# Optimization experiments

Measured on AMD Instinct MI355X. Metric: run time of the kernel, lower is better.

The kernel has to match this reference:

```python
import jax, jax.numpy as jnp
import numpy as np

HID = 128
N_USER = 50000
N_MERCH = 50000
D_IN = 64


def _glorot(key, shape):
    fan_in = shape[1]
    return jax.random.normal(key, shape, dtype=jnp.float32) / jnp.sqrt(jnp.float32(fan_in))


def _sage(x_src, x_dst, ei, Wl, bl, Wr, n_dst):
    # PyG SAGEConv: lin_l(mean_aggr(x_j)) + lin_r(x_dst)
    row, col = ei[0], ei[1]
    agg = jax.ops.segment_sum(x_src[row], col, num_segments=n_dst)
    cnt = jax.ops.segment_sum(jnp.ones((ei.shape[1],), x_src.dtype), col, num_segments=n_dst)
    mean = agg / jnp.maximum(cnt, 1.0)[:, None]
    return mean @ Wl.T + bl + x_dst @ Wr.T


def setup_inputs() -> dict:
    key = jax.random.key(0)
    ks = jax.random.split(key, 24)
    inp = {
        "x_user": jax.random.normal(ks[0], (N_USER, D_IN), dtype=jnp.float32),
        "x_merchant": jax.random.normal(ks[1], (N_MERCH, D_IN), dtype=jnp.float32),
        "edge_um": jax.random.randint(ks[2], (2, 1000000), 0, 50000, dtype=jnp.int64),
        "edge_mu": jax.random.randint(ks[3], (2, 1000000), 0, 50000, dtype=jnp.int64),
        "target_edge_index": jax.random.randint(ks[4], (2, 500000), 0, 50000, dtype=jnp.int64),
        # layer 1, edge type user->merchant (src=user D_IN, dst=merchant D_IN)
        "W1_um_l": _glorot(ks[5], (HID, D_IN)), "b1_um_l": jnp.zeros((HID,), jnp.float32),
        "W1_um_r": _glorot(ks[6], (HID, D_IN)),
        # layer 1, edge type merchant->user
        "W1_mu_l": _glorot(ks[7], (HID, D_IN)), "b1_mu_l": jnp.zeros((HID,), jnp.float32),
        "W1_mu_r": _glorot(ks[8], (HID, D_IN)),
        # layer 2 (hidden -> hidden)
        "W2_um_l": _glorot(ks[9], (HID, HID)), "b2_um_l": jnp.zeros((HID,), jnp.float32),
        "W2_um_r": _glorot(ks[10], (HID, HID)),
        "W2_mu_l": _glorot(ks[11], (HID, HID)), "b2_mu_l": jnp.zeros((HID,), jnp.float32),
        "W2_mu_r": _glorot(ks[12], (HID, HID)),
        # edge classifier MLP
        "Wc1": _glorot(ks[13], (HID, 2 * HID)), "bc1": jnp.zeros((HID,), jnp.float32),
        "Wc2": _glorot(ks[14], (1, HID)), "bc2": jnp.zeros((1,), jnp.float32),
    }
    return inp


def reference(x_user, x_merchant, edge_um, edge_mu, target_edge_index,
              W1_um_l, b1_um_l, W1_um_r, W1_mu_l, b1_mu_l, W1_mu_r,
              W2_um_l, b2_um_l, W2_um_r, W2_mu_l, b2_mu_l, W2_mu_r,
              Wc1, bc1, Wc2, bc2):
    # layer 1 (to_hetero: each dst type aggregates its single incoming edge type)
    h_m = jax.nn.relu(_sage(x_user, x_merchant, edge_um, W1_um_l, b1_um_l, W1_um_r, N_MERCH))
    h_u = jax.nn.relu(_sage(x_merchant, x_user, edge_mu, W1_mu_l, b1_mu_l, W1_mu_r, N_USER))
    # layer 2 (no relu)
    z_m = _sage(h_u, h_m, edge_um, W2_um_l, b2_um_l, W2_um_r, N_MERCH)
    z_u = _sage(h_m, h_u, edge_mu, W2_mu_l, b2_mu_l, W2_mu_r, N_USER)
    # edge classifier: sender_type='user', receiver_type='merchant'
    row, col = target_edge_index[0], target_edge_index[1]
    z = jnp.concatenate([z_u[row], z_m[col]], axis=-1)  # [E_t, 2*HID]
    z = jax.nn.relu(z @ Wc1.T + bc1)
    z = z @ Wc2.T + bc2
    return z.reshape(-1)
```

## Files before the change

### kernel.cpp

```cpp
#include <hip/hip_runtime.h>
#include <hip/hip_bf16.h>
#include <stdint.h>

#define N_USERC  50000
#define N_MERCHC 50000
#define NEC      1000000
#define NTC      500000

#define NB    196
#define BCAP  8192
#define ECHUNK 2048
#define BPT   489

#define PREP_BKT   (2 * BPT)
#define PREP_CASTX (PREP_BKT + 3125)
#define PREP_CASTW (PREP_CASTX + 16)
#define PREP_TOT   (PREP_CASTW + 257)

typedef unsigned short ushortT;
typedef __attribute__((ext_vector_type(8))) short short8;
typedef __attribute__((ext_vector_type(8))) unsigned short ushort8;
typedef __attribute__((ext_vector_type(4))) float f32x4;
typedef __attribute__((ext_vector_type(2))) float f32x2;

__device__ __forceinline__ unsigned short f2bf(float f)
{
    const unsigned u = __float_as_uint(f);
    const unsigned r = u + 0x7fffu + ((u >> 16) & 1u);
    return (unsigned short)(r >> 16);
}
__device__ __forceinline__ float bfhi(unsigned u) { return __uint_as_float(u & 0xffff0000u); }
__device__ __forceinline__ float bflo(unsigned u) { return __uint_as_float(u << 16); }

__device__ __forceinline__ void acc8p(f32x2* a, const uint4 v)
{
    a[0] += (f32x2){bflo(v.x), bfhi(v.x)};
    a[1] += (f32x2){bflo(v.y), bfhi(v.y)};
    a[2] += (f32x2){bflo(v.z), bfhi(v.z)};
    a[3] += (f32x2){bflo(v.w), bfhi(v.w)};
}

__global__ __launch_bounds__(256) void k_prep(
    const float* __restrict__ xu, const float* __restrict__ xm,
    ushortT* __restrict__ A1u, ushortT* __restrict__ A1m,
    const float* __restrict__ W1um_l, const float* __restrict__ W1um_r,
    const float* __restrict__ W1mu_l, const float* __restrict__ W1mu_r,
    ushortT* __restrict__ B1m, ushortT* __restrict__ B1u,
    const float* __restrict__ Wc1,
    const float* __restrict__ W2mu_l, const float* __restrict__ W2mu_r,
    const float* __restrict__ W2um_l, const float* __restrict__ W2um_r,
    const float* __restrict__ bc1,
    const float* __restrict__ b2mu_l, const float* __restrict__ b2um_l,
    ushortT* __restrict__ WPQ, float* __restrict__ bPQ,
    const int* __restrict__ rowA, const int* __restrict__ colA,
    const int* __restrict__ rowB, const int* __restrict__ colB,
    uint32_t* __restrict__ gcnt, uint32_t* __restrict__ bktA, uint32_t* __restrict__ bktB)
{
    __shared__ uint32_t hist[NB], base[NB], cur[NB];
    const int bid = blockIdx.x;
    const int tx = threadIdx.x;

    if (bid < PREP_BKT) {
        const int type = (bid >= BPT) ? 1 : 0;
        const int cb = bid - type * BPT;
        const int* col = type ? colB : colA;
        const int* row = type ? rowB : rowA;
        uint32_t* bkt = type ? bktB : bktA;
        uint32_t* gc = gcnt + type * NB;

        const int e0 = cb * ECHUNK;
        const int e1 = (e0 + ECHUNK < NEC) ? e0 + ECHUNK : NEC;

        for (int i = tx; i < NB; i += 256) { hist[i] = 0; cur[i] = 0; }
        __syncthreads();

        int cols[8];
#pragma unroll
        for (int q = 0; q < 8; ++q) {
            const int i = e0 + tx + q * 256;
            int c = -1;
            if (i < e1) { c = col[i]; atomicAdd(&hist[c >> 8], 1u); }
            cols[q] = c;
        }
        __syncthreads();
        for (int i = tx; i < NB; i += 256)
            base[i] = atomicAdd(&gc[i], hist[i]);
        __syncthreads();
#pragma unroll
        for (int q = 0; q < 8; ++q) {
            const int i = e0 + tx + q * 256;
            if (i < e1) {
                const int c = cols[q];
                const int b = c >> 8;
                const uint32_t p = base[b] + atomicAdd(&cur[b], 1u);
                if (p < BCAP)
                    bkt[(size_t)b * BCAP + p] = ((uint32_t)(c & 255) << 16) | (uint32_t)row[i];
            }
        }
    } else if (bid < PREP_CASTX) {
        const int idx = (bid - PREP_BKT) * 256 + tx;
        if (idx >= 800000) return;
        const int which = idx / 400000;
        const int rem = idx - which * 400000;
        const int row = rem >> 3;
        const int c8 = rem & 7;
        const float* x = which ? xm : xu;
        ushortT* A = which ? A1m : A1u;
        const float4 v0 = *(const float4*)(x + (size_t)row * 64 + c8 * 8);
        const float4 v1 = *(const float4*)(x + (size_t)row * 64 + c8 * 8 + 4);
        ushort8 o;
        o[0] = f2bf(v0.x); o[1] = f2bf(v0.y); o[2] = f2bf(v0.z); o[3] = f2bf(v0.w);
        o[4] = f2bf(v1.x); o[5] = f2bf(v1.y); o[6] = f2bf(v1.z); o[7] = f2bf(v1.w);
        *(ushort8*)(A + (size_t)row * 128 + 64 + c8 * 8) = o;
    } else if (bid < PREP_CASTW) {
        const int idx = (bid - PREP_CASTX) * 256 + tx;
        if (idx >= 4096) return;
        const int which = idx >> 11;
        const int rem = idx & 2047;
        const int n = rem >> 4;
        const int k0 = (rem & 15) * 8;
        const float* Wl = which ? W1mu_l : W1um_l;
        const float* Wr = which ? W1mu_r : W1um_r;
        const float* src = (k0 < 64) ? Wl + (size_t)n * 64 + k0
                                     : Wr + (size_t)n * 64 + (k0 - 64);
        const float4 v0 = *(const float4*)src;
        const float4 v1 = *(const float4*)(src + 4);
        ushort8 o;
        o[0] = f2bf(v0.x); o[1] = f2bf(v0.y); o[2] = f2bf(v0.z); o[3] = f2bf(v0.w);
        o[4] = f2bf(v1.x); o[5] = f2bf(v1.y); o[6] = f2bf(v1.z); o[7] = f2bf(v1.w);
        ushortT* O = which ? B1u : B1m;
        *(ushort8*)(O + (size_t)n * 128 + k0) = o;
    } else {
        const int idx = (bid - PREP_CASTW) * 256 + tx;
        if (idx < 65536) {
            const int q = idx >> 15;
            const int j = (idx >> 8) & 127;
            const int k = idx & 255;
            const int kk = k & 127;
            const float* W2 = q ? (k < 128 ? W2um_l : W2um_r)
                                : (k < 128 ? W2mu_l : W2mu_r);
            const float* wrow = Wc1 + (size_t)j * 256 + q * 128;
            float s = 0.f;
            for (int i = 0; i < 128; ++i)
                s = fmaf(wrow[i], W2[(size_t)i * 128 + kk], s);
            WPQ[idx] = f2bf(s);
        } else if (idx < 65536 + 256) {
            const int r = idx - 65536;
            const int q = r >> 7, j = r & 127;
            const float* wrow = Wc1 + (size_t)j * 256 + q * 128;
            const float* b2 = q ? b2um_l : b2mu_l;
            float s = (q == 0) ? bc1[j] : 0.f;
            for (int i = 0; i < 128; ++i) s = fmaf(wrow[i], b2[i], s);
            bPQ[r] = s;
        }
    }
}

__global__ __launch_bounds__(512) void k_bplace(
    const uint32_t* __restrict__ gcnt,
    const uint32_t* __restrict__ bktA, const uint32_t* __restrict__ bktB,
    int* __restrict__ off_um, int* __restrict__ srcs_um,
    int* __restrict__ off_mu, int* __restrict__ srcs_mu)
{
    __shared__ uint32_t sb[256], cnt[256], loff[256], cur[256];
    const int type = (blockIdx.x >= NB) ? 1 : 0;
    const int b = blockIdx.x - type * NB;
    const uint32_t* bkt = (type ? bktB : bktA) + (size_t)b * BCAP;
    int* offp = type ? off_mu : off_um;
    int* srcs = type ? srcs_mu : srcs_um;
    const int t = threadIdx.x;

    if (t < 256) sb[t] = (t < NB) ? gcnt[type * NB + t] : 0;
    for (int d = 1; d < 256; d <<= 1) {
        __syncthreads();
        uint32_t a = 0;
        if (t < 256 && t >= d) a = sb[t - d];
        __syncthreads();
        if (t < 256) sb[t] += a;
    }
    __syncthreads();
    const int n = (int)gcnt[type * NB + b];
    const uint32_t gbase = sb[b] - (uint32_t)n;
    if (blockIdx.x == 0 && t == 0)  off_um[N_MERCHC] = NEC;
    if (blockIdx.x == NB && t == 0) off_mu[N_USERC] = NEC;

    if (t < 256) { cnt[t] = 0; cur[t] = 0; }
    __syncthreads();
    for (int i = t; i < n; i += 512)
        atomicAdd(&cnt[bkt[i] >> 16], 1u);
    __syncthreads();
    if (t < 256) loff[t] = cnt[t];
    for (int d = 1; d < 256; d <<= 1) {
        __syncthreads();
        uint32_t a = 0;
        if (t < 256 && t >= d) a = loff[t - d];
        __syncthreads();
        if (t < 256) loff[t] += a;
    }
    __syncthreads();
    if (t < 256) loff[t] -= cnt[t];
    __syncthreads();
    if (t < 256) {
        const int dst0 = b << 8;
        if (dst0 + t < N_USERC) offp[dst0 + t] = (int)(gbase + loff[t]);
    }
    for (int i = t; i < n; i += 512) {
        const uint32_t v = bkt[i];
        const uint32_t ld = v >> 16;
        const uint32_t p = gbase + loff[ld] + atomicAdd(&cur[ld], 1u);
        srcs[p] = (int)(v & 0xFFFFu);
    }
}

template <int D>
__global__ __launch_bounds__(256) void k_agg(
    const ushortT* __restrict__ gA, const int* __restrict__ offsA,
    const int* __restrict__ srcsA, ushortT* __restrict__ oA,
    const ushortT* __restrict__ gB, const int* __restrict__ offsB,
    const int* __restrict__ srcsB, ushortT* __restrict__ oB, int ndst)
{
    constexpr int LPE = D / 8;
    constexpr int EPW = 64 / LPE;
    constexpr int UNR = (D == 128) ? 8 : 4;
    constexpr int STR = 2 * D;
    constexpr unsigned RB = 4 * D;
    const int half = gridDim.x >> 1;
    const int type = (blockIdx.x >= half) ? 1 : 0;
    const int cb = blockIdx.x - type * half;
    const ushortT* g = type ? gB : gA;
    const int* offs  = type ? offsB : offsA;
    const int* srcs  = type ? srcsB : srcsA;
    ushortT* om      = type ? oB : oA;

    const int wid = cb * 4 + (threadIdx.x >> 6);
    if (wid >= ndst) return;
    const int lane = threadIdx.x & 63;
    const int sub  = lane / LPE;
    const int c4   = lane % LPE;

    const int b = offs[wid], e = offs[wid + 1];
    const int deg = e - b;
    const char* gDc = (const char*)(g + D) + c4 * 16;

    f32x2 a0[4], a1[4];
#pragma unroll
    for (int j = 0; j < 4; ++j) { a0[j] = (f32x2){0.f, 0.f}; a1[j] = (f32x2){0.f, 0.f}; }

    if (deg <= 64) {
        const int sidx = (b + lane < NEC) ? b + lane : NEC - 1;
        const int src_l = srcs[sidx];
        for (int t0 = 0; t0 < deg; t0 += UNR * EPW) {
            uint4 v[UNR];
#pragma unroll
            for (int r = 0; r < UNR; ++r) {
                const int j = t0 + r * EPW + sub;
                const int s = __shfl(src_l, j);
                v[r] = (uint4){0u, 0u, 0u, 0u};
                if (j < deg)
                    v[r] = *(const uint4*)(gDc + (unsigned)s * RB);
            }
            __builtin_amdgcn_sched_barrier(0);
#pragma unroll
            for (int r = 0; r < UNR; ++r)
                acc8p((r & 1) ? a1 : a0, v[r]);
        }
    } else {
        int i = b + sub;
        for (; i + EPW < e; i += 2 * EPW) {
            const uint4 v0 = *(const uint4*)(gDc + (unsigned)srcs[i] * RB);
            const uint4 v1 = *(const uint4*)(gDc + (unsigned)srcs[i + EPW] * RB);
            acc8p(a0, v0);
            acc8p(a1, v1);
        }
        if (i < e) {
            const uint4 v = *(const uint4*)(gDc + (unsigned)srcs[i] * RB);
            acc8p(a0, v);
        }
    }

    float r[8];
#pragma unroll
    for (int j = 0; j < 4; ++j) {
        r[2 * j]     = a0[j].x + a1[j].x;
        r[2 * j + 1] = a0[j].y + a1[j].y;
    }
#pragma unroll
    for (int m = LPE; m < 64; m <<= 1) {
#pragma unroll
        for (int j = 0; j < 8; ++j) r[j] += __shfl_xor(r[j], m);
    }
    if (sub == 0) {
        const float inv = 1.0f / (float)(deg > 1 ? deg : 1);
        ushort8 o;
#pragma unroll
        for (int j = 0; j < 8; ++j) o[j] = f2bf(r[j] * inv);
        *(ushort8*)(om + (size_t)wid * STR + c4 * 8) = o;
    }
}

template <int K, bool RELU>
__device__ __forceinline__ void mfma_gemm_body(
    int cb, float (*lds)[16][132],
    const ushortT* __restrict__ A, const ushortT* __restrict__ Bw,
    const float* __restrict__ bias,
    ushortT* __restrict__ Obf, int OS, int OO, int M)
{
    const int tx = threadIdx.x;
    const int wid = tx >> 6;
    const int lane = tx & 63;
    const int ln = lane & 15;
    const int quad = lane >> 4;
    const int m0 = cb * 256 + wid * 64;

    const ushortT* ap[4];
#pragma unroll
    for (int i = 0; i < 4; ++i) {
        int arow = m0 + i * 16 + ln; if (arow >= M) arow = M - 1;
        ap[i] = A + (size_t)arow * K + quad * 8;
    }

    f32x4 acc[4][8];
#pragma unroll
    for (int i = 0; i < 4; ++i)
#pragma unroll
        for (int nt = 0; nt < 8; ++nt) acc[i][nt] = (f32x4){0.f, 0.f, 0.f, 0.f};

#pragma unroll
    for (int kc = 0; kc < K / 32; ++kc) {
        short8 a[4];
#pragma unroll
        for (int i = 0; i < 4; ++i) a[i] = *(const short8*)(ap[i] + kc * 32);
#pragma unroll
        for (int nt = 0; nt < 8; ++nt) {
            const short8 b = *(const short8*)(Bw + (size_t)(nt * 16 + ln) * K + kc * 32 + quad * 8);
#pragma unroll
            for (int i = 0; i < 4; ++i)
                acc[i][nt] = __builtin_amdgcn_mfma_f32_16x16x32_bf16(a[i], b, acc[i][nt], 0, 0, 0);
        }
    }

    float (*t)[132] = lds[wid];
#pragma unroll
    for (int i = 0; i < 4; ++i) {
#pragma unroll
        for (int nt = 0; nt < 8; ++nt) {
            const float bv = bias[nt * 16 + ln];
#pragma unroll
            for (int r = 0; r < 4; ++r) {
                float v = acc[i][nt][r] + bv;
                if (RELU) v = fmaxf(v, 0.f);
                t[quad * 4 + r][nt * 16 + ln] = v;
            }
        }
#pragma unroll
        for (int p = 0; p < 4; ++p) {
            const int row = p * 4 + quad;
            const int gr = m0 + i * 16 + row;
            if (gr < M) {
                const float4 v0 = *(const float4*)&t[row][ln * 8];
                const float4 v1 = *(const float4*)&t[row][ln * 8 + 4];
                ushort8 o;
                o[0] = f2bf(v0.x); o[1] = f2bf(v0.y); o[2] = f2bf(v0.z); o[3] = f2bf(v0.w);
                o[4] = f2bf(v1.x); o[5] = f2bf(v1.y); o[6] = f2bf(v1.z); o[7] = f2bf(v1.w);
                *(ushort8*)(Obf + (size_t)gr * OS + OO + ln * 8) = o;
            }
        }
    }
}

template <int K, bool RELU>
__global__ __launch_bounds__(256) void k_mfma_gemm2(
    const ushortT* __restrict__ Aa, const ushortT* __restrict__ Bwa,
    const float* __restrict__ biasa, ushortT* __restrict__ Oa, int OSa, int OOa, int Ma,
    const ushortT* __restrict__ Ab, const ushortT* __restrict__ Bwb,
    const float* __restrict__ biasb, ushortT* __restrict__ Ob, int OSb, int OOb, int Mb,
    int gridA)
{
    __shared__ float lds[4][16][132];
    if ((int)blockIdx.x < gridA)
        mfma_gemm_body<K, RELU>(blockIdx.x, lds, Aa, Bwa, biasa, Oa, OSa, OOa, Ma);
    else
        mfma_gemm_body<K, RELU>(blockIdx.x - gridA, lds, Ab, Bwb, biasb, Ob, OSb, OOb, Mb);
}

__global__ __launch_bounds__(256) void k_edge_bf(
    const ushortT* __restrict__ P, const ushortT* __restrict__ Q,
    const int* __restrict__ er, const int* __restrict__ ec,
    const float* __restrict__ wc2, const float* __restrict__ bc2,
    float* __restrict__ out, int nt)
{
    const int lane = threadIdx.x & 63;
    const int sub = lane >> 4;
    const int c8 = lane & 15;
    const int wid = (int)((blockIdx.x * blockDim.x + threadIdx.x) >> 6);
    const int e0 = wid * 4 + sub;
    if (e0 >= nt) return;

    const float4 w0 = ((const float4*)wc2)[c8 * 2];
    const float4 w1 = ((const float4*)wc2)[c8 * 2 + 1];
    const int r = er[e0], c = ec[e0];
    const uint4 pv = *(const uint4*)(P + (size_t)r * 128 + c8 * 8);
    const uint4 qv = *(const uint4*)(Q + (size_t)c * 128 + c8 * 8);
    float s = fmaxf(bflo(pv.x) + bflo(qv.x), 0.f) * w0.x
            + fmaxf(bfhi(pv.x) + bfhi(qv.x), 0.f) * w0.y
            + fmaxf(bflo(pv.y) + bflo(qv.y), 0.f) * w0.z
            + fmaxf(bfhi(pv.y) + bfhi(qv.y), 0.f) * w0.w
            + fmaxf(bflo(pv.z) + bflo(qv.z), 0.f) * w1.x
            + fmaxf(bfhi(pv.z) + bfhi(qv.z), 0.f) * w1.y
            + fmaxf(bflo(pv.w) + bflo(qv.w), 0.f) * w1.z
            + fmaxf(bfhi(pv.w) + bfhi(qv.w), 0.f) * w1.w;
    s += __shfl_xor(s, 1);
    s += __shfl_xor(s, 2);
    s += __shfl_xor(s, 4);
    s += __shfl_xor(s, 8);
    if (c8 == 0) out[e0] = s + bc2[0];
}

extern "C" void kernel_launch(void* const* d_in, const int* in_sizes, int n_in,
                              void* d_out, int out_size, void* d_ws, size_t ws_size,
                              hipStream_t stream)
{
    const float* x_user  = (const float*)d_in[0];
    const float* x_merch = (const float*)d_in[1];
    const int*   e_um    = (const int*)d_in[2];
    const int*   e_mu    = (const int*)d_in[3];
    const int*   tgt     = (const int*)d_in[4];
    const float* W1_um_l = (const float*)d_in[5];
    const float* b1_um_l = (const float*)d_in[6];
    const float* W1_um_r = (const float*)d_in[7];
    const float* W1_mu_l = (const float*)d_in[8];
    const float* b1_mu_l = (const float*)d_in[9];
    const float* W1_mu_r = (const float*)d_in[10];
    const float* W2_um_l = (const float*)d_in[11];
    const float* b2_um_l = (const float*)d_in[12];
    const float* W2_um_r = (const float*)d_in[13];
    const float* W2_mu_l = (const float*)d_in[14];
    const float* b2_mu_l = (const float*)d_in[15];
    const float* W2_mu_r = (const float*)d_in[16];
    const float* Wc1     = (const float*)d_in[17];
    const float* bc1     = (const float*)d_in[18];
    const float* Wc2     = (const float*)d_in[19];
    const float* bc2     = (const float*)d_in[20];
    float* out = (float*)d_out;

    uint32_t* B = (uint32_t*)d_ws;
    size_t pos = 0;
    auto take = [&](size_t n) { size_t p = pos; pos += (n + 63) & ~(size_t)63; return p; };

    uint32_t* gcnt = (uint32_t*)(B + take(2 * NB));
    const size_t cnt_words = pos;
    int* off_um  = (int*)(B + take(N_MERCHC + 1));
    int* srcs_um = (int*)(B + take(NEC));
    int* off_mu  = (int*)(B + take(N_USERC + 1));
    int* srcs_mu = (int*)(B + take(NEC));
    ushortT* A1u = (ushortT*)(B + take((size_t)N_USERC  * 128 / 2));
    ushortT* A1m = (ushortT*)(B + take((size_t)N_MERCHC * 128 / 2));
    ushortT* A2u = (ushortT*)(B + take((size_t)N_USERC  * 256 / 2));
    ushortT* A2m = (ushortT*)(B + take((size_t)N_MERCHC * 256 / 2));
    ushortT* B1m = (ushortT*)(B + take(8192));
    ushortT* B1u = (ushortT*)(B + take(8192));
    ushortT* WPQ = (ushortT*)(B + take(32768));
    float*   bPQ = (float*)(B + take(256));

    uint32_t* bktA = (uint32_t*)A2m;
    uint32_t* bktB = bktA + (size_t)NB * BCAP;
    ushortT* Pbf = A1u;
    ushortT* Qbf = A1m;
    (void)ws_size; (void)in_sizes; (void)n_in; (void)out_size;

    hipMemsetAsync(d_ws, 0, cnt_words * sizeof(uint32_t), stream);

    k_prep<<<PREP_TOT, 256, 0, stream>>>(
        x_user, x_merch, A1u, A1m,
        W1_um_l, W1_um_r, W1_mu_l, W1_mu_r, B1m, B1u,
        Wc1, W2_mu_l, W2_mu_r, W2_um_l, W2_um_r, bc1, b2_mu_l, b2_um_l, WPQ, bPQ,
        e_um, e_um + NEC, e_mu, e_mu + NEC, gcnt, bktA, bktB);

    k_bplace<<<2 * NB, 512, 0, stream>>>(gcnt, bktA, bktB,
                                         off_um, srcs_um, off_mu, srcs_mu);

    const int agrid = 50000 / 4;
    k_agg<64><<<2 * agrid, 256, 0, stream>>>(
        A1u, off_um, srcs_um, A1m,
        A1m, off_mu, srcs_mu, A1u, N_MERCHC);

    const int ggrid = (50000 + 255) / 256;
    k_mfma_gemm2<128, true><<<2 * ggrid, 256, 0, stream>>>(
        A1m, B1m, b1_um_l, A2m, 256, 128, N_MERCHC,
        A1u, B1u, b1_mu_l, A2u, 256, 128, N_USERC, ggrid);

    k_agg<128><<<2 * agrid, 256, 0, stream>>>(
        A2u, off_um, srcs_um, A2m,
        A2m, off_mu, srcs_mu, A2u, N_MERCHC);

    k_mfma_gemm2<256, false><<<2 * ggrid, 256, 0, stream>>>(
        A2u, WPQ,         bPQ,       Pbf, 128, 0, N_USERC,
        A2m, WPQ + 32768, bPQ + 128, Qbf, 128, 0, N_MERCHC, ggrid);

    const int cgrid = (NTC + 15) / 16;
    k_edge_bf<<<cgrid, 256, 0, stream>>>(Pbf, Qbf, tgt, tgt + NTC, Wc2, bc2, out, NTC);
}
```

Measured before the change: 348.5 us.

## Bucket target edges by user into CSR so edge classifier reuses P rows

```diff
diff --git a/kernel.cpp b/kernel.cpp
--- a/kernel.cpp
+++ b/kernel.cpp
@@ -9,10 +9,12 @@
 
 #define NB    196
 #define BCAP  8192
+#define TCAP  4096
 #define ECHUNK 2048
 #define BPT   489
-
-#define PREP_BKT   (2 * BPT)
+#define BPTT  245
+
+#define PREP_BKT   (2 * BPT + BPTT)
 #define PREP_CASTX (PREP_BKT + 3125)
 #define PREP_CASTW (PREP_CASTX + 16)
 #define PREP_TOT   (PREP_CASTW + 257)
@@ -38,6 +40,19 @@
     a[1] += (f32x2){bflo(v.y), bfhi(v.y)};
     a[2] += (f32x2){bflo(v.z), bfhi(v.z)};
     a[3] += (f32x2){bflo(v.w), bfhi(v.w)};
+}
+
+__device__ __forceinline__ float edot8(const uint4 pv, const uint4 qv,
+                                       const float4 w0, const float4 w1)
+{
+    return fmaxf(bflo(pv.x) + bflo(qv.x), 0.f) * w0.x
+         + fmaxf(bfhi(pv.x) + bfhi(qv.x), 0.f) * w0.y
+         + fmaxf(bflo(pv.y) + bflo(qv.y), 0.f) * w0.z
+         + fmaxf(bfhi(pv.y) + bfhi(qv.y), 0.f) * w0.w
+         + fmaxf(bflo(pv.z) + bflo(qv.z), 0.f) * w1.x
+         + fmaxf(bfhi(pv.z) + bfhi(qv.z), 0.f) * w1.y
+         + fmaxf(bflo(pv.w) + bflo(qv.w), 0.f) * w1.z
+         + fmaxf(bfhi(pv.w) + bfhi(qv.w), 0.f) * w1.w;
 }
 
 __global__ __launch_bounds__(256) void k_prep(
@@ -54,22 +69,26 @@
     ushortT* __restrict__ WPQ, float* __restrict__ bPQ,
     const int* __restrict__ rowA, const int* __restrict__ colA,
     const int* __restrict__ rowB, const int* __restrict__ colB,
-    uint32_t* __restrict__ gcnt, uint32_t* __restrict__ bktA, uint32_t* __restrict__ bktB)
+    const int* __restrict__ tgr, const int* __restrict__ tgc,
+    uint32_t* __restrict__ gcnt, uint32_t* __restrict__ bktA, uint32_t* __restrict__ bktB,
+    uint32_t* __restrict__ bktTlo, uint32_t* __restrict__ bktThi)
 {
     __shared__ uint32_t hist[NB], base[NB], cur[NB];
     const int bid = blockIdx.x;
     const int tx = threadIdx.x;
 
     if (bid < PREP_BKT) {
-        const int type = (bid >= BPT) ? 1 : 0;
-        const int cb = bid - type * BPT;
-        const int* col = type ? colB : colA;
-        const int* row = type ? rowB : rowA;
-        uint32_t* bkt = type ? bktB : bktA;
+        const int type = (bid >= 2 * BPT) ? 2 : (bid >= BPT ? 1 : 0);
+        const int cb = bid - (type == 2 ? 2 * BPT : type * BPT);
+        const int* col = (type == 2) ? tgr : (type ? colB : colA);
+        const int* row = (type == 2) ? tgc : (type ? rowB : rowA);
+        uint32_t* bklo = (type == 2) ? bktTlo : (type ? bktB : bktA);
         uint32_t* gc = gcnt + type * NB;
+        const int nE  = (type == 2) ? NTC : NEC;
+        const int cap = (type == 2) ? TCAP : BCAP;
 
         const int e0 = cb * ECHUNK;
-        const int e1 = (e0 + ECHUNK < NEC) ? e0 + ECHUNK : NEC;
+        const int e1 = (e0 + ECHUNK < nE) ? e0 + ECHUNK : nE;
 
         for (int i = tx; i < NB; i += 256) { hist[i] = 0; cur[i] = 0; }
         __syncthreads();
@@ -93,8 +112,11 @@
                 const int c = cols[q];
                 const int b = c >> 8;
                 const uint32_t p = base[b] + atomicAdd(&cur[b], 1u);
-                if (p < BCAP)
-                    bkt[(size_t)b * BCAP + p] = ((uint32_t)(c & 255) << 16) | (uint32_t)row[i];
+                if (p < (uint32_t)cap) {
+                    const uint32_t idx = (uint32_t)b * cap + p;
+                    bklo[idx] = ((uint32_t)(c & 255) << 16) | (uint32_t)row[i];
+                    if (type == 2) bktThi[idx] = (uint32_t)i;
+                }
             }
         }
     } else if (bid < PREP_CASTX) {
@@ -159,15 +181,17 @@
 __global__ __launch_bounds__(512) void k_bplace(
     const uint32_t* __restrict__ gcnt,
     const uint32_t* __restrict__ bktA, const uint32_t* __restrict__ bktB,
+    const uint32_t* __restrict__ bktTlo, const uint32_t* __restrict__ bktThi,
     int* __restrict__ off_um, int* __restrict__ srcs_um,
-    int* __restrict__ off_mu, int* __restrict__ srcs_mu)
+    int* __restrict__ off_mu, int* __restrict__ srcs_mu,
+    int* __restrict__ offT, int2* __restrict__ payT)
 {
     __shared__ uint32_t sb[256], cnt[256], loff[256], cur[256];
-    const int type = (blockIdx.x >= NB) ? 1 : 0;
+    const int type = (blockIdx.x >= 2 * NB) ? 2 : (blockIdx.x >= NB ? 1 : 0);
     const int b = blockIdx.x - type * NB;
-    const uint32_t* bkt = (type ? bktB : bktA) + (size_t)b * BCAP;
-    int* offp = type ? off_mu : off_um;
-    int* srcs = type ? srcs_mu : srcs_um;
+    const int cap = (type == 2) ? TCAP : BCAP;
+    const uint32_t* bkt = ((type == 2) ? bktTlo : (type ? bktB : bktA)) + (size_t)b * cap;
+    int* offp = (type == 2) ? offT : (type ? off_mu : off_um);
     const int t = threadIdx.x;
 
     if (t < 256) sb[t] = (t < NB) ? gcnt[type * NB + t] : 0;
@@ -181,8 +205,9 @@
     __syncthreads();
     const int n = (int)gcnt[type * NB + b];
     const uint32_t gbase = sb[b] - (uint32_t)n;
-    if (blockIdx.x == 0 && t == 0)  off_um[N_MERCHC] = NEC;
-    if (blockIdx.x == NB && t == 0) off_mu[N_USERC] = NEC;
+    if (blockIdx.x == 0 && t == 0)      off_um[N_MERCHC] = NEC;
+    if (blockIdx.x == NB && t == 0)     off_mu[N_USERC] = NEC;
+    if (blockIdx.x == 2 * NB && t == 0) offT[N_USERC] = NTC;
 
     if (t < 256) { cnt[t] = 0; cur[t] = 0; }
     __syncthreads();
@@ -204,11 +229,22 @@
         const int dst0 = b << 8;
         if (dst0 + t < N_USERC) offp[dst0 + t] = (int)(gbase + loff[t]);
     }
-    for (int i = t; i < n; i += 512) {
-        const uint32_t v = bkt[i];
-        const uint32_t ld = v >> 16;
-        const uint32_t p = gbase + loff[ld] + atomicAdd(&cur[ld], 1u);
-        srcs[p] = (int)(v & 0xFFFFu);
+    if (type < 2) {
+        int* srcs = type ? srcs_mu : srcs_um;
+        for (int i = t; i < n; i += 512) {
+            const uint32_t v = bkt[i];
+            const uint32_t ld = v >> 16;
+            const uint32_t p = gbase + loff[ld] + atomicAdd(&cur[ld], 1u);
+            srcs[p] = (int)(v & 0xFFFFu);
+        }
+    } else {
+        const uint32_t* hi = bktThi + (size_t)b * cap;
+        for (int i = t; i < n; i += 512) {
+            const uint32_t v = bkt[i];
+            const uint32_t ld = v >> 16;
+            const uint32_t p = gbase + loff[ld] + atomicAdd(&cur[ld], 1u);
+            payT[p] = (int2){(int)(v & 0xFFFFu), (int)hi[i]};
+        }
     }
 }
 
@@ -383,37 +419,36 @@
         mfma_gemm_body<K, RELU>(blockIdx.x - gridA, lds, Ab, Bwb, biasb, Ob, OSb, OOb, Mb);
 }
 
-__global__ __launch_bounds__(256) void k_edge_bf(
+__global__ __launch_bounds__(256) void k_edge_csr(
     const ushortT* __restrict__ P, const ushortT* __restrict__ Q,
-    const int* __restrict__ er, const int* __restrict__ ec,
+    const int* __restrict__ offT, const int2* __restrict__ payT,
     const float* __restrict__ wc2, const float* __restrict__ bc2,
-    float* __restrict__ out, int nt)
-{
+    float* __restrict__ out)
+{
+    const int wid = (int)((blockIdx.x * blockDim.x + threadIdx.x) >> 6);
+    if (wid >= N_USERC) return;
     const int lane = threadIdx.x & 63;
     const int sub = lane >> 4;
     const int c8 = lane & 15;
-    const int wid = (int)((blockIdx.x * blockDim.x + threadIdx.x) >> 6);
-    const int e0 = wid * 4 + sub;
-    if (e0 >= nt) return;
+
+    const int b = offT[wid], e = offT[wid + 1];
+    if (b == e) return;
 
     const float4 w0 = ((const float4*)wc2)[c8 * 2];
     const float4 w1 = ((const float4*)wc2)[c8 * 2 + 1];
-    const int r = er[e0], c = ec[e0];
-    const uint4 pv = *(const uint4*)(P + (size_t)r * 128 + c8 * 8);
-    const uint4 qv = *(const uint4*)(Q + (size_t)c * 128 + c8 * 8);
-    float s = fmaxf(bflo(pv.x) + bflo(qv.x), 0.f) * w0.x
-            + fmaxf(bfhi(pv.x) + bfhi(qv.x), 0.f) * w0.y
-            + fmaxf(bflo(pv.y) + bflo(qv.y), 0.f) * w0.z
-            + fmaxf(bfhi(pv.y) + bfhi(qv.y), 0.f) * w0.w
-            + fmaxf(bflo(pv.z) + bflo(qv.z), 0.f) * w1.x
-            + fmaxf(bfhi(pv.z) + bfhi(qv.z), 0.f) * w1.y
-            + fmaxf(bflo(pv.w) + bflo(qv.w), 0.f) * w1.z
-            + fmaxf(bfhi(pv.w) + bfhi(qv.w), 0.f) * w1.w;
-    s += __shfl_xor(s, 1);
-    s += __shfl_xor(s, 2);
-    s += __shfl_xor(s, 4);
-    s += __shfl_xor(s, 8);
-    if (c8 == 0) out[e0] = s + bc2[0];
+    const float bb = bc2[0];
+    const uint4 pv = *(const uint4*)(P + (size_t)wid * 128 + c8 * 8);
+
+    for (int i = b + sub; i < e; i += 4) {
+        const int2 pe = payT[i];
+        const uint4 qv = *(const uint4*)(Q + (size_t)pe.x * 128 + c8 * 8);
+        float s = edot8(pv, qv, w0, w1);
+        s += __shfl_xor(s, 1);
+        s += __shfl_xor(s, 2);
+        s += __shfl_xor(s, 4);
+        s += __shfl_xor(s, 8);
+        if (c8 == 0) out[pe.y] = s + bb;
+    }
 }
 
 extern "C" void kernel_launch(void* const* d_in, const int* in_sizes, int n_in,
@@ -447,12 +482,14 @@
     size_t pos = 0;
     auto take = [&](size_t n) { size_t p = pos; pos += (n + 63) & ~(size_t)63; return p; };
 
-    uint32_t* gcnt = (uint32_t*)(B + take(2 * NB));
+    uint32_t* gcnt = (uint32_t*)(B + take(3 * NB));
     const size_t cnt_words = pos;
     int* off_um  = (int*)(B + take(N_MERCHC + 1));
     int* srcs_um = (int*)(B + take(NEC));
     int* off_mu  = (int*)(B + take(N_USERC + 1));
     int* srcs_mu = (int*)(B + take(NEC));
+    int* offT    = (int*)(B + take(N_USERC + 1));
+    int2* payT   = (int2*)(B + take(2 * (size_t)NTC));
     ushortT* A1u = (ushortT*)(B + take((size_t)N_USERC  * 128 / 2));
     ushortT* A1m = (ushortT*)(B + take((size_t)N_MERCHC * 128 / 2));
     ushortT* A2u = (ushortT*)(B + take((size_t)N_USERC  * 256 / 2));
@@ -462,8 +499,10 @@
     ushortT* WPQ = (ushortT*)(B + take(32768));
     float*   bPQ = (float*)(B + take(256));
 
-    uint32_t* bktA = (uint32_t*)A2m;
-    uint32_t* bktB = bktA + (size_t)NB * BCAP;
+    uint32_t* bktA   = (uint32_t*)A2m;
+    uint32_t* bktB   = bktA + (size_t)NB * BCAP;
+    uint32_t* bktTlo = bktB + (size_t)NB * BCAP;
+    uint32_t* bktThi = bktTlo + (size_t)NB * TCAP;
     ushortT* Pbf = A1u;
     ushortT* Qbf = A1m;
     (void)ws_size; (void)in_sizes; (void)n_in; (void)out_size;
@@ -474,10 +513,11 @@
         x_user, x_merch, A1u, A1m,
         W1_um_l, W1_um_r, W1_mu_l, W1_mu_r, B1m, B1u,
         Wc1, W2_mu_l, W2_mu_r, W2_um_l, W2_um_r, bc1, b2_mu_l, b2_um_l, WPQ, bPQ,
-        e_um, e_um + NEC, e_mu, e_mu + NEC, gcnt, bktA, bktB);
-
-    k_bplace<<<2 * NB, 512, 0, stream>>>(gcnt, bktA, bktB,
-                                         off_um, srcs_um, off_mu, srcs_mu);
+        e_um, e_um + NEC, e_mu, e_mu + NEC, tgt, tgt + NTC,
+        gcnt, bktA, bktB, bktTlo, bktThi);
+
+    k_bplace<<<3 * NB, 512, 0, stream>>>(gcnt, bktA, bktB, bktTlo, bktThi,
+                                         off_um, srcs_um, off_mu, srcs_mu, offT, payT);
 
     const int agrid = 50000 / 4;
     k_agg<64><<<2 * agrid, 256, 0, stream>>>(
@@ -497,6 +537,6 @@
         A2u, WPQ,         bPQ,       Pbf, 128, 0, N_USERC,
         A2m, WPQ + 32768, bPQ + 128, Qbf, 128, 0, N_MERCHC, ggrid);
 
-    const int cgrid = (NTC + 15) / 16;
-    k_edge_bf<<<cgrid, 256, 0, stream>>>(Pbf, Qbf, tgt, tgt + NTC, Wc2, bc2, out, NTC);
-}
+    const int cgrid = (N_USERC + 3) / 4;
+    k_edge_csr<<<cgrid, 256, 0, stream>>>(Pbf, Qbf, offT, payT, Wc2, bc2, out);
+}
```

After: 362.7 us. 1.04x slower.

## Bucket target edges by user row to localize classifier gathers

Applied to the files above, without the earlier changes.

```diff
diff --git a/kernel.cpp b/kernel.cpp
--- a/kernel.cpp
+++ b/kernel.cpp
@@ -9,10 +9,12 @@
 
 #define NB    196
 #define BCAP  8192
+#define TCAP  4096
 #define ECHUNK 2048
 #define BPT   489
-
-#define PREP_BKT   (2 * BPT)
+#define BPTT  245
+
+#define PREP_BKT   (2 * BPT + BPTT)
 #define PREP_CASTX (PREP_BKT + 3125)
 #define PREP_CASTW (PREP_CASTX + 16)
 #define PREP_TOT   (PREP_CASTW + 257)
@@ -38,6 +40,19 @@
     a[1] += (f32x2){bflo(v.y), bfhi(v.y)};
     a[2] += (f32x2){bflo(v.z), bfhi(v.z)};
     a[3] += (f32x2){bflo(v.w), bfhi(v.w)};
+}
+
+__device__ __forceinline__ float edot8(const uint4 pv, const uint4 qv,
+                                       const float4 w0, const float4 w1)
+{
+    return fmaxf(bflo(pv.x) + bflo(qv.x), 0.f) * w0.x
+         + fmaxf(bfhi(pv.x) + bfhi(qv.x), 0.f) * w0.y
+         + fmaxf(bflo(pv.y) + bflo(qv.y), 0.f) * w0.z
+         + fmaxf(bfhi(pv.y) + bfhi(qv.y), 0.f) * w0.w
+         + fmaxf(bflo(pv.z) + bflo(qv.z), 0.f) * w1.x
+         + fmaxf(bfhi(pv.z) + bfhi(qv.z), 0.f) * w1.y
+         + fmaxf(bflo(pv.w) + bflo(qv.w), 0.f) * w1.z
+         + fmaxf(bfhi(pv.w) + bfhi(qv.w), 0.f) * w1.w;
 }
 
 __global__ __launch_bounds__(256) void k_prep(
@@ -54,22 +69,26 @@
     ushortT* __restrict__ WPQ, float* __restrict__ bPQ,
     const int* __restrict__ rowA, const int* __restrict__ colA,
     const int* __restrict__ rowB, const int* __restrict__ colB,
-    uint32_t* __restrict__ gcnt, uint32_t* __restrict__ bktA, uint32_t* __restrict__ bktB)
+    const int* __restrict__ tgr, const int* __restrict__ tgc,
+    uint32_t* __restrict__ gcnt, uint32_t* __restrict__ bktA, uint32_t* __restrict__ bktB,
+    uint64_t* __restrict__ bktT)
 {
     __shared__ uint32_t hist[NB], base[NB], cur[NB];
     const int bid = blockIdx.x;
     const int tx = threadIdx.x;
 
     if (bid < PREP_BKT) {
-        const int type = (bid >= BPT) ? 1 : 0;
-        const int cb = bid - type * BPT;
-        const int* col = type ? colB : colA;
-        const int* row = type ? rowB : rowA;
+        const int type = (bid >= 2 * BPT) ? 2 : (bid >= BPT ? 1 : 0);
+        const int cb = bid - (type == 2 ? 2 * BPT : type * BPT);
+        const int* col = (type == 2) ? tgr : (type ? colB : colA);
+        const int* row = (type == 2) ? tgc : (type ? rowB : rowA);
         uint32_t* bkt = type ? bktB : bktA;
         uint32_t* gc = gcnt + type * NB;
+        const int nE  = (type == 2) ? NTC : NEC;
+        const int cap = (type == 2) ? TCAP : BCAP;
 
         const int e0 = cb * ECHUNK;
-        const int e1 = (e0 + ECHUNK < NEC) ? e0 + ECHUNK : NEC;
+        const int e1 = (e0 + ECHUNK < nE) ? e0 + ECHUNK : nE;
 
         for (int i = tx; i < NB; i += 256) { hist[i] = 0; cur[i] = 0; }
         __syncthreads();
@@ -93,8 +112,15 @@
                 const int c = cols[q];
                 const int b = c >> 8;
                 const uint32_t p = base[b] + atomicAdd(&cur[b], 1u);
-                if (p < BCAP)
-                    bkt[(size_t)b * BCAP + p] = ((uint32_t)(c & 255) << 16) | (uint32_t)row[i];
+                if (p < (uint32_t)cap) {
+                    if (type == 2)
+                        bktT[(size_t)b * TCAP + p] = ((uint64_t)(c & 255) << 40)
+                                                   | ((uint64_t)(uint32_t)i << 20)
+                                                   | (uint64_t)(uint32_t)row[i];
+                    else
+                        bkt[(size_t)b * BCAP + p] =
+                            ((uint32_t)(c & 255) << 16) | (uint32_t)row[i];
+                }
             }
         }
     } else if (bid < PREP_CASTX) {
@@ -383,37 +409,40 @@
         mfma_gemm_body<K, RELU>(blockIdx.x - gridA, lds, Ab, Bwb, biasb, Ob, OSb, OOb, Mb);
 }
 
-__global__ __launch_bounds__(256) void k_edge_bf(
+__global__ __launch_bounds__(256) void k_edge_bkt(
     const ushortT* __restrict__ P, const ushortT* __restrict__ Q,
-    const int* __restrict__ er, const int* __restrict__ ec,
+    const uint32_t* __restrict__ gcnt, const uint64_t* __restrict__ bktT,
     const float* __restrict__ wc2, const float* __restrict__ bc2,
-    float* __restrict__ out, int nt)
-{
+    float* __restrict__ out)
+{
+    const int b  = blockIdx.x >> 4;
+    const int sl = blockIdx.x & 15;
+    int n = (int)gcnt[2 * NB + b];
+    if (n > TCAP) n = TCAP;
+    const uint64_t* bkt = bktT + (size_t)b * TCAP;
     const int lane = threadIdx.x & 63;
-    const int sub = lane >> 4;
+    const int slot = ((threadIdx.x >> 6) << 2) + (lane >> 4);
     const int c8 = lane & 15;
-    const int wid = (int)((blockIdx.x * blockDim.x + threadIdx.x) >> 6);
-    const int e0 = wid * 4 + sub;
-    if (e0 >= nt) return;
 
     const float4 w0 = ((const float4*)wc2)[c8 * 2];
     const float4 w1 = ((const float4*)wc2)[c8 * 2 + 1];
-    const int r = er[e0], c = ec[e0];
-    const uint4 pv = *(const uint4*)(P + (size_t)r * 128 + c8 * 8);
-    const uint4 qv = *(const uint4*)(Q + (size_t)c * 128 + c8 * 8);
-    float s = fmaxf(bflo(pv.x) + bflo(qv.x), 0.f) * w0.x
-            + fmaxf(bfhi(pv.x) + bfhi(qv.x), 0.f) * w0.y
-            + fmaxf(bflo(pv.y) + bflo(qv.y), 0.f) * w0.z
-            + fmaxf(bfhi(pv.y) + bfhi(qv.y), 0.f) * w0.w
-            + fmaxf(bflo(pv.z) + bflo(qv.z), 0.f) * w1.x
-            + fmaxf(bfhi(pv.z) + bfhi(qv.z), 0.f) * w1.y
-            + fmaxf(bflo(pv.w) + bflo(qv.w), 0.f) * w1.z
-            + fmaxf(bfhi(pv.w) + bfhi(qv.w), 0.f) * w1.w;
-    s += __shfl_xor(s, 1);
-    s += __shfl_xor(s, 2);
-    s += __shfl_xor(s, 4);
-    s += __shfl_xor(s, 8);
-    if (c8 == 0) out[e0] = s + bc2[0];
+    const float bb = bc2[0];
+    const ushortT* Pb = P + (size_t)(b << 8) * 128;
+
+    for (int i = sl + (slot << 4); i < n; i += 256) {
+        const uint64_t v = bkt[i];
+        const int c   = (int)(v & 0xFFFFFu);
+        const int eid = (int)((v >> 20) & 0xFFFFFu);
+        const int rl  = (int)(v >> 40);
+        const uint4 pv = *(const uint4*)(Pb + (size_t)rl * 128 + c8 * 8);
+        const uint4 qv = *(const uint4*)(Q + (size_t)c * 128 + c8 * 8);
+        float s = edot8(pv, qv, w0, w1);
+        s += __shfl_xor(s, 1);
+        s += __shfl_xor(s, 2);
+        s += __shfl_xor(s, 4);
+        s += __shfl_xor(s, 8);
+        if (c8 == 0) out[eid] = s + bb;
+    }
 }
 
 extern "C" void kernel_launch(void* const* d_in, const int* in_sizes, int n_in,
@@ -447,12 +476,13 @@
     size_t pos = 0;
     auto take = [&](size_t n) { size_t p = pos; pos += (n + 63) & ~(size_t)63; return p; };
 
-    uint32_t* gcnt = (uint32_t*)(B + take(2 * NB));
+    uint32_t* gcnt = (uint32_t*)(B + take(3 * NB));
     const size_t cnt_words = pos;
     int* off_um  = (int*)(B + take(N_MERCHC + 1));
     int* srcs_um = (int*)(B + take(NEC));
     int* off_mu  = (int*)(B + take(N_USERC + 1));
     int* srcs_mu = (int*)(B + take(NEC));
+    uint64_t* bktT = (uint64_t*)(B + take((size_t)NB * TCAP * 2));
     ushortT* A1u = (ushortT*)(B + take((size_t)N_USERC  * 128 / 2));
     ushortT* A1m = (ushortT*)(B + take((size_t)N_MERCHC * 128 / 2));
     ushortT* A2u = (ushortT*)(B + take((size_t)N_USERC  * 256 / 2));
@@ -474,7 +504,8 @@
         x_user, x_merch, A1u, A1m,
         W1_um_l, W1_um_r, W1_mu_l, W1_mu_r, B1m, B1u,
         Wc1, W2_mu_l, W2_mu_r, W2_um_l, W2_um_r, bc1, b2_mu_l, b2_um_l, WPQ, bPQ,
-        e_um, e_um + NEC, e_mu, e_mu + NEC, gcnt, bktA, bktB);
+        e_um, e_um + NEC, e_mu, e_mu + NEC, tgt, tgt + NTC,
+        gcnt, bktA, bktB, bktT);
 
     k_bplace<<<2 * NB, 512, 0, stream>>>(gcnt, bktA, bktB,
                                          off_um, srcs_um, off_mu, srcs_mu);
@@ -497,6 +528,5 @@
         A2u, WPQ,         bPQ,       Pbf, 128, 0, N_USERC,
         A2m, WPQ + 32768, bPQ + 128, Qbf, 128, 0, N_MERCHC, ggrid);
 
-    const int cgrid = (NTC + 15) / 16;
-    k_edge_bf<<<cgrid, 256, 0, stream>>>(Pbf, Qbf, tgt, tgt + NTC, Wc2, bc2, out, NTC);
-}
+    k_edge_bkt<<<NB * 16, 256, 0, stream>>>(Pbf, Qbf, gcnt, bktT, Wc2, bc2, out);
+}
```

New measurement: 359.6 us. 3.2% more time.
